# Performance work log

Hardware: AMD Instinct MI355X
Metric: run time of the kernel (lower is better)

The kernel has to match this reference:

```python
import jax, jax.numpy as jnp
import numpy as np

DIM = 192
NUM_HEADS = 6
WS = (2, 8, 8)          # (wd, wh, ww)
SHIFT = (1, 4, 4)
B, D, H, W = 2, 4, 128, 128
N_WIN_TOK = WS[0] * WS[1] * WS[2]   # 128
NW = (D // WS[0]) * (H // WS[1]) * (W // WS[2])  # 512 windows per sample


def _rel_pos_index(ws):
    d, h, w = ws
    coords = np.stack(np.meshgrid(np.arange(d), np.arange(h), np.arange(w), indexing='ij'))
    cf = coords.reshape(3, -1)
    rel = (cf[:, :, None] - cf[:, None, :]).transpose(1, 2, 0).astype(np.int64)
    rel[:, :, 0] += d - 1
    rel[:, :, 1] += h - 1
    rel[:, :, 2] += w - 1
    rel[:, :, 0] *= (2 * h - 1) * (2 * w - 1)
    rel[:, :, 1] *= 2 * w - 1
    return rel.sum(-1)  # (N, N)

REL_IDX = _rel_pos_index(WS)


def _sine_pos(HW, num_pos_feats, temperature=10000.0):
    # matches get_sine_position_encoding(normalize=True)
    scale = 2 * np.pi
    eps = 1e-6
    ones = np.ones((1, HW[0], HW[1]), np.float32)
    y = ones.cumsum(1)
    x = ones.cumsum(2)
    y = y / (y[:, -1:, :] + eps) * scale
    x = x / (x[:, :, -1:] + eps) * scale
    i = np.arange(num_pos_feats, dtype=np.float32)
    dim_t = temperature ** (2.0 * np.floor(i / 2) / num_pos_feats)
    px = x[:, :, :, None] / dim_t
    py = y[:, :, :, None] / dim_t
    px = np.stack((np.sin(px[..., 0::2]), np.cos(px[..., 1::2])), axis=4).reshape(1, HW[0], HW[1], -1)
    py = np.stack((np.sin(py[..., 0::2]), np.cos(py[..., 1::2])), axis=4).reshape(1, HW[0], HW[1], -1)
    pos = np.concatenate((py, px), axis=3)  # (1, H, W, 2*npf)
    return pos.reshape(1, HW[0] * HW[1], -1)

POS_BIAS = _sine_pos((WS[1], WS[2]), DIM // 2)  # (1, 64, DIM)


def _ln(x, w, b):
    mu = x.mean(-1, keepdims=True)
    var = x.var(-1, keepdims=True)
    return (x - mu) / jnp.sqrt(var + 1e-5) * w + b


def _qkv(x, w, b):
    B_, N, C = x.shape
    y = (x @ w.T + b).reshape(B_, N, 3, NUM_HEADS, C // NUM_HEADS).transpose(2, 0, 3, 1, 4)
    return y[0], y[1], y[2]  # each (B_, h, N, hd)


def _attn(q, k, v, mask, rpb=None):
    # q,k,v: (B_, h, N, hd); mask: (nW, N, N) or None; rpb: (h, N, N) or None
    scale = q.shape[-1] ** -0.5
    a = jnp.einsum('bhnd,bhmd->bhnm', q * scale, k)
    if rpb is not None:
        a = a + rpb[None]
    if mask is not None:
        B_, h, N, _ = a.shape
        nW = mask.shape[0]
        a = (a.reshape(B_ // nW, nW, h, N, N) + mask[None, :, None]).reshape(B_, h, N, N)
    a = jax.nn.softmax(a, axis=-1)
    out = jnp.einsum('bhnm,bhmd->bhnd', a, v)
    B_, h, N, hd = out.shape
    return out.transpose(0, 2, 1, 3).reshape(B_, N, h * hd)


def setup_inputs() -> dict:
    key = jax.random.key(0)
    ks = jax.random.split(key, 8)
    C = DIM
    hid = int(C * 2.0)
    f = lambda k, shp: jax.random.normal(k, shp, jnp.float32) * 0.02
    tbl = (2 * WS[0] - 1) * (2 * WS[1] - 1) * (2 * WS[2] - 1)
    return {
        'x': jax.random.normal(ks[0], (B, D, H, W, C), jnp.float32),
        'mask_matrix': jnp.zeros((NW, N_WIN_TOK, N_WIN_TOK), jnp.float32),
        'norm1_w': jnp.ones((C,), jnp.float32), 'norm1_b': jnp.zeros((C,), jnp.float32),
        'qkv_self_w': f(ks[1], (3 * C, C)), 'qkv_self_b': jnp.zeros((3 * C,), jnp.float32),
        'qkv_mut_w': f(ks[2], (3 * C, C)), 'qkv_mut_b': jnp.zeros((3 * C,), jnp.float32),
        'rpb_table': f(ks[3], (tbl, NUM_HEADS)),
        'proj_w': f(ks[4], (C, 2 * C)), 'proj_b': jnp.zeros((C,), jnp.float32),
        'norm2_w': jnp.ones((C,), jnp.float32), 'norm2_b': jnp.zeros((C,), jnp.float32),
        'fc11_w': f(ks[5], (hid, C)), 'fc11_b': jnp.zeros((hid,), jnp.float32),
        'fc12_w': f(ks[6], (hid, C)), 'fc12_b': jnp.zeros((hid,), jnp.float32),
        'fc2_w': f(ks[7], (C, hid)), 'fc2_b': jnp.zeros((C,), jnp.float32),
    }


def reference(x, mask_matrix, norm1_w, norm1_b, qkv_self_w, qkv_self_b,
              qkv_mut_w, qkv_mut_b, rpb_table, proj_w, proj_b,
              norm2_w, norm2_b, fc11_w, fc11_b, fc12_w, fc12_b, fc2_w, fc2_b):
    Bb, Dd, Hh, Ww_, C = x.shape
    wd, wh, ww = WS
    N = wd * wh * ww
    Nh = N // 2

    # ---- part1: windowed mutual+self attention with cyclic shift ----
    h1 = _ln(x, norm1_w, norm1_b)
    sh = jnp.roll(h1, (-SHIFT[0], -SHIFT[1], -SHIFT[2]), axis=(1, 2, 3))
    # window_partition -> (B*nW, N, C)
    xw = sh.reshape(Bb, Dd // wd, wd, Hh // wh, wh, Ww_ // ww, ww, C)
    xw = xw.transpose(0, 1, 3, 5, 2, 4, 6, 7).reshape(-1, N, C)

    # self-attention with relative position bias
    q, k, v = _qkv(xw, qkv_self_w, qkv_self_b)
    rpb = rpb_table[REL_IDX.reshape(-1)].reshape(N, N, NUM_HEADS).transpose(2, 0, 1)
    x_self = _attn(q, k, v, mask_matrix[:, :N, :N], rpb)  # (B_, N, C)

    # mutual attention (no relative bias), sine positional bias added to input
    pos = jnp.tile(jnp.asarray(POS_BIAS, x.dtype), (1, 2, 1))  # (1, N, C)
    q, k, v = _qkv(xw + pos, qkv_mut_w, qkv_mut_b)
    q1, q2 = q[:, :, :Nh], q[:, :, Nh:]
    k1, k2 = k[:, :, :Nh], k[:, :, Nh:]
    v1, v2 = v[:, :, :Nh], v[:, :, Nh:]
    m2 = mask_matrix[:, :Nh, :Nh]
    x1 = _attn(q2, k1, v1, m2)  # frame2 queries attend frame1
    x2 = _attn(q1, k2, v2, m2)
    x_out = jnp.concatenate([jnp.concatenate([x1, x2], axis=1), x_self], axis=2)  # (B_, N, 2C)
    xp = x_out @ proj_w.T + proj_b  # (B_, N, C)

    # window_reverse + roll back
    rev = xp.reshape(Bb, Dd // wd, Hh // wh, Ww_ // ww, wd, wh, ww, C)
    rev = rev.transpose(0, 1, 4, 2, 5, 3, 6, 7).reshape(Bb, Dd, Hh, Ww_, C)
    rev = jnp.roll(rev, SHIFT, axis=(1, 2, 3))
    x = x + rev

    # ---- part2: GEGLU MLP ----
    h2 = _ln(x, norm2_w, norm2_b)
    mlp = (jax.nn.gelu(h2 @ fc11_w.T + fc11_b, approximate=False) * (h2 @ fc12_w.T + fc12_b)) @ fc2_w.T + fc2_b
    return x + mlp
```

## Files before the change

kernel.cpp:

```cpp
#include <hip/hip_runtime.h>
#include <hip/hip_bf16.h>

typedef __hip_bfloat16 bf16;
typedef __attribute__((ext_vector_type(8))) short short8;
typedef __attribute__((ext_vector_type(4))) float f32x4;

#define NTOKENS 131072
#define MFMA __builtin_amdgcn_mfma_f32_16x16x32_bf16

static constexpr size_t A_OFF    = 0;
static constexpr size_t Q_OFF    = A_OFF   + (size_t)NTOKENS*192*2;
static constexpr size_t O_OFF    = Q_OFF   + (size_t)NTOKENS*576*2;
static constexpr size_t POS_OFF  = O_OFF   + (size_t)NTOKENS*384*2;
static constexpr size_t PB_OFF   = POS_OFF + (size_t)128*192*4;
static constexpr size_t RPBF_OFF = PB_OFF  + (size_t)128*576*4;
static constexpr size_t MSKF_OFF = RPBF_OFF+ (size_t)6*128*128*2;
static constexpr size_t WB_OFF   = MSKF_OFF+ (size_t)512*128*128*2;
static constexpr size_t WQS_E = 0, WQM_E = 110592, WPR_E = 221184,
                        W11_E = 294912, W12_E = 368640, W2_E = 442368, WTOT = 516096;

__device__ __forceinline__ float u2f(unsigned int ubits) {
    union { unsigned int i; float f; } c; c.i = ubits << 16; return c.f;
}
__device__ __forceinline__ unsigned pkbf(float a, float b) {
    unsigned ua = (unsigned)__bfloat16_as_ushort(__float2bfloat16(a));
    unsigned ub = (unsigned)__bfloat16_as_ushort(__float2bfloat16(b));
    return ua | (ub << 16);
}
__device__ __forceinline__ unsigned swz(unsigned b) { return b ^ (((b >> 9) & 1) << 5); }
__device__ __forceinline__ short8 u4s8(uint4 v) { union { uint4 u; short8 s; } c; c.u = v; return c.s; }

__device__ __forceinline__ void gl16(const bf16* g, void* l) {
    __builtin_amdgcn_global_load_lds(
        (const __attribute__((address_space(1))) void*)g,
        (__attribute__((address_space(3))) void*)l, 16, 0, 0);
}

__global__ __launch_bounds__(256) void cvtw_kernel(
    const float* __restrict__ a, const float* __restrict__ b, const float* __restrict__ c,
    const float* __restrict__ d, const float* __restrict__ e, const float* __restrict__ f,
    bf16* __restrict__ out) {
    int i = blockIdx.x * 256 + threadIdx.x;
    const float* src; int off;
    if      (i < (int)WQM_E) { src = a; off = (int)WQS_E; }
    else if (i < (int)WPR_E) { src = b; off = (int)WQM_E; }
    else if (i < (int)W11_E) { src = c; off = (int)WPR_E; }
    else if (i < (int)W12_E) { src = d; off = (int)W11_E; }
    else if (i < (int)W2_E)  { src = e; off = (int)W12_E; }
    else if (i < (int)WTOT)  { src = f; off = (int)W2_E; }
    else return;
    out[i] = __float2bfloat16(src[i - off]);
}

__global__ __launch_bounds__(256) void pos_kernel(float* __restrict__ pos) {
    int idx = blockIdx.x * 256 + threadIdx.x;
    if (idx >= 128 * 192) return;
    int t = idx / 192, c = idx - t * 192;
    int s = t & 63;
    int hh = s >> 3, ww = s & 7;
    const float twopi = 6.2831853071795864f;
    float coord = (c < 96) ? (float)(hh + 1) : (float)(ww + 1);
    coord = coord / (8.0f + 1e-6f) * twopi;
    int f = (c < 96) ? c : c - 96;
    float dimt = powf(10000.0f, (float)(2 * (f >> 1)) / 96.0f);
    float v = coord / dimt;
    pos[idx] = (f & 1) ? cosf(v) : sinf(v);
}

__global__ __launch_bounds__(256) void pbias_kernel(const float* __restrict__ pos,
                                                    const bf16* __restrict__ Wm,
                                                    const float* __restrict__ bqm,
                                                    float* __restrict__ PB) {
    int idx = blockIdx.x * 256 + threadIdx.x;
    if (idx >= 128 * 576) return;
    int t = idx / 576, n = idx - t * 576;
    const float* pp = pos + t * 192;
    const bf16* wp = Wm + (size_t)n * 192;
    float acc = bqm[n];
    for (int k = 0; k < 192; ++k) acc += pp[k] * __bfloat162float(wp[k]);
    PB[idx] = acc;
}

__global__ __launch_bounds__(256) void rpbF_kernel(const float* __restrict__ tbl,
                                                   bf16* __restrict__ rpbF) {
    int idx = blockIdx.x * 256 + threadIdx.x;
    if (idx >= 6 * 32 * 128 * 4) return;
    int jr = idx & 3;
    int i = (idx >> 2) & 127;
    int jq = (idx >> 9) & 31;
    int h = idx >> 14;
    int j = jq * 4 + jr;
    int di = i >> 6, hi = (i >> 3) & 7, wi = i & 7;
    int dj = j >> 6, hj = (j >> 3) & 7, wj = j & 7;
    int t = (di - dj + 1) * 225 + (hi - hj + 7) * 15 + (wi - wj + 7);
    rpbF[idx] = __float2bfloat16(tbl[t * 6 + h]);
}

__global__ __launch_bounds__(256) void mskF_kernel(const float* __restrict__ mask,
                                                   bf16* __restrict__ mskF) {
    int idx = blockIdx.x * 256 + threadIdx.x;
    int widx = idx >> 12;
    int rem = idx & 4095;
    int i = rem >> 5, jq = rem & 31;
    float4 v = *reinterpret_cast<const float4*>(mask + ((size_t)widx << 14) + i * 128 + jq * 4);
    uint2 o;
    o.x = pkbf(v.x, v.y);
    o.y = pkbf(v.z, v.w);
    *reinterpret_cast<uint2*>(mskF + ((size_t)widx << 14) + (jq * 128 + i) * 4) = o;
}

template <int PART>
__global__ __launch_bounds__(256) void ln_kernel(const float* __restrict__ xin,
                                                 const float* __restrict__ w,
                                                 const float* __restrict__ b,
                                                 bf16* __restrict__ out) {
    int tok = blockIdx.x * 4 + (threadIdx.x >> 6);
    int lane = threadIdx.x & 63;
    const float* xp = xin + (size_t)tok * 192;
    float x0 = xp[lane], x1 = xp[lane + 64], x2 = xp[lane + 128];
    float s = x0 + x1 + x2;
    float ss = x0 * x0 + x1 * x1 + x2 * x2;
    for (int off = 32; off; off >>= 1) {
        s += __shfl_xor(s, off);
        ss += __shfl_xor(ss, off);
    }
    float mean = s * (1.0f / 192.0f);
    float var = ss * (1.0f / 192.0f) - mean * mean;
    float rstd = rsqrtf(var + 1e-5f);
    size_t obase;
    if (PART) {
        int bb = tok >> 16;
        int rem = tok & 65535;
        int d = rem >> 14;
        int hw = rem & 16383;
        int hh = hw >> 7, w2 = hw & 127;
        int sd = (d + 3) & 3;
        int sh = (hh + 124) & 127;
        int sw = (w2 + 124) & 127;
        int win = ((bb * 2 + (sd >> 1)) * 16 + (sh >> 3)) * 16 + (sw >> 3);
        int t = ((sd & 1) << 6) | ((sh & 7) << 3) | (sw & 7);
        obase = ((size_t)win * 128 + t) * 192;
    } else {
        obase = (size_t)tok * 192;
    }
    out[obase + lane]       = __float2bfloat16((x0 - mean) * rstd * w[lane] + b[lane]);
    out[obase + lane + 64]  = __float2bfloat16((x1 - mean) * rstd * w[lane + 64] + b[lane + 64]);
    out[obase + lane + 128] = __float2bfloat16((x2 - mean) * rstd * w[lane + 128] + b[lane + 128]);
}

template <int MODE, int BIAS>
__global__ __launch_bounds__(256) void mgemm(
    const bf16* __restrict__ Ab, int K, int nb,
    const bf16* __restrict__ W1, const float* __restrict__ B1,
    const bf16* __restrict__ W2, const float* __restrict__ B2,
    const float* __restrict__ resid,
    void* __restrict__ outp, void* __restrict__ outp2) {
    constexpr bool DUAL = (MODE == 3 || MODE == 5);
    __shared__ __align__(16) unsigned char AsB[2][16384];
    __shared__ __align__(16) unsigned char WsB[2][8192];
    __shared__ __align__(16) unsigned char Ws2B[DUAL ? 2 : 1][DUAL ? 8192 : 16];

    int total = gridDim.x;
    int bid = blockIdx.x;
    int lin = (bid & 7) * (total >> 3) + (bid >> 3);
    int mb = lin / nb, nbk = lin - mb * nb;
    int m0 = mb << 7, n0 = nbk << 6;
    int tid = threadIdx.x;
    int w = tid >> 6, l = tid & 63;
    int wr = w >> 1, wc = w & 1;
    int lr = l & 15, lg = l >> 4;

    f32x4 acc[4][2] = {};
    f32x4 acc2[4][2] = {};

    auto stage = [&](int buf, int kc) {
        int k0 = kc << 6;
#pragma unroll
        for (int it = 0; it < 4; ++it) {
            int idx = it * 256 + tid;
            int row = idx >> 3, gs = idx & 7;
            int gsrc = gs ^ (((row >> 2) & 1) << 1);
            gl16(Ab + (size_t)(m0 + row) * K + k0 + gsrc * 8, &AsB[buf][idx * 16]);
        }
#pragma unroll
        for (int it = 0; it < 2; ++it) {
            int idx = it * 256 + tid;
            int row = idx >> 3, gs = idx & 7;
            int gsrc = gs ^ (((row >> 2) & 1) << 1);
            gl16(W1 + (size_t)(n0 + row) * K + k0 + gsrc * 8, &WsB[buf][idx * 16]);
            if (DUAL)
                gl16(W2 + (size_t)(n0 + row) * K + k0 + gsrc * 8, &Ws2B[buf][idx * 16]);
        }
    };

    int nK = K >> 6;
    stage(0, 0);
    __syncthreads();
    for (int kc = 0; kc < nK; ++kc) {
        int cur = kc & 1;
        if (kc + 1 < nK) stage(cur ^ 1, kc + 1);
        const unsigned char* as = AsB[cur];
        const unsigned char* wsb = WsB[cur];
        const unsigned char* ws2 = Ws2B[DUAL ? cur : 0];
#pragma unroll
        for (int ks = 0; ks < 2; ++ks) {
            short8 af[4], wf[2], wf2[2];
#pragma unroll
            for (int rb = 0; rb < 4; ++rb)
                af[rb] = *reinterpret_cast<const short8*>(
                    &as[swz((wr * 64 + rb * 16 + lr) * 128 + ks * 64 + lg * 16)]);
#pragma unroll
            for (int cb = 0; cb < 2; ++cb) {
                wf[cb] = *reinterpret_cast<const short8*>(
                    &wsb[swz((wc * 32 + cb * 16 + lr) * 128 + ks * 64 + lg * 16)]);
                if (DUAL)
                    wf2[cb] = *reinterpret_cast<const short8*>(
                        &ws2[swz((wc * 32 + cb * 16 + lr) * 128 + ks * 64 + lg * 16)]);
            }
#pragma unroll
            for (int rb = 0; rb < 4; ++rb)
#pragma unroll
                for (int cb = 0; cb < 2; ++cb) {
                    acc[rb][cb] = MFMA(af[rb], wf[cb], acc[rb][cb], 0, 0, 0);
                    if (DUAL) acc2[rb][cb] = MFMA(af[rb], wf2[cb], acc2[rb][cb], 0, 0, 0);
                }
        }
        __syncthreads();
    }

    if (MODE == 5) {
        bf16* eb1 = (bf16*)AsB[0];
        bf16* eb2 = (bf16*)AsB[1];
        float pbv[4][2][4];
#pragma unroll
        for (int rb = 0; rb < 4; ++rb)
#pragma unroll
            for (int r = 0; r < 4; ++r) {
                int ml = wr * 64 + rb * 16 + lg * 4 + r;
#pragma unroll
                for (int cb = 0; cb < 2; ++cb)
                    pbv[rb][cb][r] = resid[(ml & 127) * 576 + n0 + wc * 32 + cb * 16 + lr];
            }
#pragma unroll
        for (int rb = 0; rb < 4; ++rb)
#pragma unroll
            for (int r = 0; r < 4; ++r) {
                int ml = wr * 64 + rb * 16 + lg * 4 + r;
#pragma unroll
                for (int cb = 0; cb < 2; ++cb) {
                    int cl = wc * 32 + cb * 16 + lr;
                    int n = n0 + cl;
                    eb1[ml * 64 + cl] = __float2bfloat16(acc[rb][cb][r] + B1[n]);
                    eb2[ml * 64 + cl] = __float2bfloat16(acc2[rb][cb][r] + pbv[rb][cb][r]);
                }
            }
        __syncthreads();
        bf16* Og  = (bf16*)outp;
        bf16* Og2 = (bf16*)outp2;
#pragma unroll
        for (int it = 0; it < 4; ++it) {
            int idx = it * 256 + tid;
            int row = idx >> 3, g = idx & 7;
            uint4 v1 = *reinterpret_cast<const uint4*>(&eb1[row * 64 + g * 8]);
            uint4 v2 = *reinterpret_cast<const uint4*>(&eb2[row * 64 + g * 8]);
            *reinterpret_cast<uint4*>(Og  + (size_t)(m0 + row) * 576 + n0 + g * 8) = v1;
            *reinterpret_cast<uint4*>(Og2 + (size_t)(m0 + row) * 576 + n0 + g * 8) = v2;
        }
    } else if (MODE == 3) {
        bf16* eb = (bf16*)AsB[0];
#pragma unroll
        for (int rb = 0; rb < 4; ++rb)
#pragma unroll
            for (int r = 0; r < 4; ++r) {
                int ml = wr * 64 + rb * 16 + lg * 4 + r;
#pragma unroll
                for (int cb = 0; cb < 2; ++cb) {
                    int cl = wc * 32 + cb * 16 + lr;
                    int n = n0 + cl;
                    float u = acc[rb][cb][r] + B1[n];
                    float v2 = acc2[rb][cb][r] + B2[n];
                    float t = u * (0.7978845608028654f + 0.0356774081363001f * u * u);
                    float g = u * v2 / (1.0f + __expf(-2.0f * t));
                    eb[ml * 64 + cl] = __float2bfloat16(g);
                }
            }
        __syncthreads();
        bf16* Og = (bf16*)outp;
#pragma unroll
        for (int it = 0; it < 4; ++it) {
            int idx = it * 256 + tid;
            int row = idx >> 3, g = idx & 7;
            uint4 v = *reinterpret_cast<const uint4*>(&eb[row * 64 + g * 8]);
            *reinterpret_cast<uint4*>(Og + (size_t)(m0 + row) * 384 + n0 + g * 8) = v;
        }
    } else {
#pragma unroll
        for (int rb = 0; rb < 4; ++rb) {
#pragma unroll
            for (int r = 0; r < 4; ++r) {
                int m = m0 + wr * 64 + rb * 16 + lg * 4 + r;
                if (MODE == 2) {
                    int win = m >> 7, t = m & 127;
                    int bb = win >> 9, rem = win & 511;
                    int sd = ((rem >> 8) << 1) | (t >> 6);
                    int sh = (((rem >> 4) & 15) << 3) | ((t >> 3) & 7);
                    int sw = ((rem & 15) << 3) | (t & 7);
                    int dq = (sd + 1) & 3;
                    int hq = (sh + 4) & 127;
                    int wq = (sw + 4) & 127;
                    size_t gb = ((((size_t)bb * 4 + dq) * 128 + hq) * 128 + wq) * 192;
                    float* Rr = (float*)outp;
#pragma unroll
                    for (int cb = 0; cb < 2; ++cb) {
                        int n = n0 + wc * 32 + cb * 16 + lr;
                        Rr[gb + n] = resid[gb + n] + acc[rb][cb][r] + B1[n];
                    }
                } else {
                    float* Og = (float*)outp;
#pragma unroll
                    for (int cb = 0; cb < 2; ++cb) {
                        int n = n0 + wc * 32 + cb * 16 + lr;
                        Og[(size_t)m * 192 + n] =
                            resid[(size_t)m * 192 + n] + acc[rb][cb][r] + B1[n];
                    }
                }
            }
        }
    }
}

__global__ __launch_bounds__(256) void attn_self(
    const bf16* __restrict__ Qb, const bf16* __restrict__ rpbF,
    const bf16* __restrict__ mskF, bf16* __restrict__ Ob, int b2) {
    __shared__ __align__(16) bf16 VtB[4096];
    __shared__ __align__(16) bf16 EpiB[4][1280];
    int bid = blockIdx.x;
    int lin = (bid & 7) * 384 + (bid >> 3);
    int widx = lin / 6, h = lin - widx * 6;
    int win = b2 * 512 + widx;
    int tid = threadIdx.x, w = tid >> 6, l = tid & 63;
    int lr = l & 15, lg = l >> 4;
    const float qscale = 0.17677669529663689f;
    size_t qbase = (size_t)widx * 128 * 576 + h * 32;

#pragma unroll
    for (int it = 0; it < 16; ++it) {
        int idx = it * 256 + tid;
        int d = idx & 31, j = idx >> 5;
        bf16 v = Qb[qbase + (size_t)j * 576 + 384 + d];
        VtB[(d * 256 + (((j >> 3) ^ (d & 7)) << 4) + (j & 7) * 2) >> 1] = v;
    }

    uint4 kf[8], qf[2];
#pragma unroll
    for (int jb = 0; jb < 8; ++jb)
        kf[jb] = *reinterpret_cast<const uint4*>(Qb + qbase + (size_t)(jb * 16 + lr) * 576 + 192 + lg * 8);
    int i0 = w * 32;
#pragma unroll
    for (int ib = 0; ib < 2; ++ib)
        qf[ib] = *reinterpret_cast<const uint4*>(Qb + qbase + (size_t)(i0 + ib * 16 + lr) * 576 + lg * 8);
    f32x4 s[8][2] = {};
#pragma unroll
    for (int jb = 0; jb < 8; ++jb)
#pragma unroll
        for (int ib = 0; ib < 2; ++ib)
            s[jb][ib] = MFMA(u4s8(kf[jb]), u4s8(qf[ib]), s[jb][ib], 0, 0, 0);

    const bf16* rpF = rpbF + (size_t)h * 16384;
    const bf16* mpF = mskF + (size_t)widx * 16384;
#pragma unroll
    for (int jb = 0; jb < 8; ++jb) {
        int jq0 = jb * 4 + lg;
#pragma unroll
        for (int ib = 0; ib < 2; ++ib) {
            int il = i0 + ib * 16 + lr;
            uint2 rv = *reinterpret_cast<const uint2*>(rpF + (jq0 * 128 + il) * 4);
            uint2 mv = *reinterpret_cast<const uint2*>(mpF + (jq0 * 128 + il) * 4);
            s[jb][ib][0] = fmaf(s[jb][ib][0], qscale, u2f(rv.x & 0xffffu) + u2f(mv.x & 0xffffu));
            s[jb][ib][1] = fmaf(s[jb][ib][1], qscale, u2f(rv.x >> 16) + u2f(mv.x >> 16));
            s[jb][ib][2] = fmaf(s[jb][ib][2], qscale, u2f(rv.y & 0xffffu) + u2f(mv.y & 0xffffu));
            s[jb][ib][3] = fmaf(s[jb][ib][3], qscale, u2f(rv.y >> 16) + u2f(mv.y >> 16));
        }
    }

    float rs[2];
    unsigned w0[2][8], w1[2][8];
#pragma unroll
    for (int ib = 0; ib < 2; ++ib) {
        float mx = -1e30f;
#pragma unroll
        for (int jb = 0; jb < 8; ++jb)
#pragma unroll
            for (int r = 0; r < 4; ++r) mx = fmaxf(mx, s[jb][ib][r]);
        mx = fmaxf(mx, __shfl_xor(mx, 16));
        mx = fmaxf(mx, __shfl_xor(mx, 32));
        float sum = 0.0f;
#pragma unroll
        for (int jb = 0; jb < 8; ++jb)
#pragma unroll
            for (int r = 0; r < 4; ++r) {
                float e = __expf(s[jb][ib][r] - mx);
                s[jb][ib][r] = e;
                sum += e;
            }
        sum += __shfl_xor(sum, 16);
        sum += __shfl_xor(sum, 32);
        rs[ib] = 1.0f / sum;
#pragma unroll
        for (int jb = 0; jb < 8; ++jb) {
            w0[ib][jb] = pkbf(s[jb][ib][0], s[jb][ib][1]);
            w1[ib][jb] = pkbf(s[jb][ib][2], s[jb][ib][3]);
        }
    }
    __syncthreads();

    f32x4 o[2][2] = {};
    int srcA = lr + 16 * (2 * (lg & 1));
    int srcB = srcA + 16;
    bool hi = ((lg >> 1) & 1) != 0;
#pragma unroll
    for (int ks = 0; ks < 4; ++ks) {
        short8 vt[2];
#pragma unroll
        for (int db = 0; db < 2; ++db) {
            int d = db * 16 + lr;
            vt[db] = *reinterpret_cast<const short8*>(
                &VtB[(d * 256 + (((ks * 4 + lg) ^ (d & 7)) << 4)) >> 1]);
        }
#pragma unroll
        for (int ib = 0; ib < 2; ++ib) {
            unsigned xa0 = (unsigned)__shfl((int)w0[ib][2 * ks], srcA, 64);
            unsigned xa1 = (unsigned)__shfl((int)w0[ib][2 * ks + 1], srcA, 64);
            unsigned xb0 = (unsigned)__shfl((int)w1[ib][2 * ks], srcA, 64);
            unsigned xb1 = (unsigned)__shfl((int)w1[ib][2 * ks + 1], srcA, 64);
            unsigned xc0 = (unsigned)__shfl((int)w0[ib][2 * ks], srcB, 64);
            unsigned xc1 = (unsigned)__shfl((int)w0[ib][2 * ks + 1], srcB, 64);
            unsigned xd0 = (unsigned)__shfl((int)w1[ib][2 * ks], srcB, 64);
            unsigned xd1 = (unsigned)__shfl((int)w1[ib][2 * ks + 1], srcB, 64);
            uint4 bfv;
            bfv.x = hi ? xa1 : xa0;
            bfv.y = hi ? xb1 : xb0;
            bfv.z = hi ? xc1 : xc0;
            bfv.w = hi ? xd1 : xd0;
            short8 pb = u4s8(bfv);
#pragma unroll
            for (int db = 0; db < 2; ++db) o[db][ib] = MFMA(vt[db], pb, o[db][ib], 0, 0, 0);
        }
    }

    bf16* eb = &EpiB[w][0];
#pragma unroll
    for (int db = 0; db < 2; ++db)
#pragma unroll
        for (int ib = 0; ib < 2; ++ib)
#pragma unroll
            for (int r = 0; r < 4; ++r) {
                int d = db * 16 + lg * 4 + r;
                int il = ib * 16 + lr;
                eb[il * 40 + d] = __float2bfloat16(o[db][ib][r] * rs[ib]);
            }
    int il2 = l >> 1, hf = l & 1;
    uint4 oa = *reinterpret_cast<const uint4*>(&eb[il2 * 40 + hf * 16]);
    uint4 ob2 = *reinterpret_cast<const uint4*>(&eb[il2 * 40 + hf * 16 + 8]);
    size_t gbase = ((size_t)win * 128 + i0 + il2) * 384 + 192 + h * 32 + hf * 16;
    *reinterpret_cast<uint4*>(Ob + gbase) = oa;
    *reinterpret_cast<uint4*>(Ob + gbase + 8) = ob2;
}

__global__ __launch_bounds__(256) void attn_mut(
    const bf16* __restrict__ Qb, const bf16* __restrict__ mskF, bf16* __restrict__ Ob,
    int b2) {
    __shared__ __align__(16) bf16 VtB[4096];
    __shared__ __align__(16) bf16 EpiB[4][1280];
    int bid = blockIdx.x;
    int lin = (bid & 7) * 384 + (bid >> 3);
    int widx = lin / 6, h = lin - widx * 6;
    int win = b2 * 512 + widx;
    int tid = threadIdx.x, w = tid >> 6, l = tid & 63;
    int lr = l & 15, lg = l >> 4;
    const float qscale = 0.17677669529663689f;
    size_t qbase = (size_t)widx * 128 * 576 + h * 32;

#pragma unroll
    for (int it = 0; it < 16; ++it) {
        int idx = it * 256 + tid;
        int d = idx & 31, j = idx >> 5;
        bf16 v = Qb[qbase + (size_t)j * 576 + 384 + d];
        VtB[(d * 256 + (((j >> 3) ^ (d & 7)) << 4) + (j & 7) * 2) >> 1] = v;
    }

    int i0 = w * 32;
    int qoff = (w < 2) ? 64 : -64;
    int koff = (w < 2) ? 0 : 64;
    uint4 kf[4], qf[2];
#pragma unroll
    for (int jb = 0; jb < 4; ++jb)
        kf[jb] = *reinterpret_cast<const uint4*>(
            Qb + qbase + (size_t)(koff + jb * 16 + lr) * 576 + 192 + lg * 8);
#pragma unroll
    for (int ib = 0; ib < 2; ++ib)
        qf[ib] = *reinterpret_cast<const uint4*>(
            Qb + qbase + (size_t)(i0 + ib * 16 + lr + qoff) * 576 + lg * 8);
    f32x4 s[4][2] = {};
#pragma unroll
    for (int jb = 0; jb < 4; ++jb)
#pragma unroll
        for (int ib = 0; ib < 2; ++ib)
            s[jb][ib] = MFMA(u4s8(kf[jb]), u4s8(qf[ib]), s[jb][ib], 0, 0, 0);

    const bf16* mpF = mskF + (size_t)widx * 16384;
    int ibase = (i0 & 63);
#pragma unroll
    for (int jb = 0; jb < 4; ++jb) {
        int jq0 = jb * 4 + lg;
#pragma unroll
        for (int ib = 0; ib < 2; ++ib) {
            int il = ibase + ib * 16 + lr;
            uint2 mv = *reinterpret_cast<const uint2*>(mpF + (jq0 * 128 + il) * 4);
            s[jb][ib][0] = fmaf(s[jb][ib][0], qscale, u2f(mv.x & 0xffffu));
            s[jb][ib][1] = fmaf(s[jb][ib][1], qscale, u2f(mv.x >> 16));
            s[jb][ib][2] = fmaf(s[jb][ib][2], qscale, u2f(mv.y & 0xffffu));
            s[jb][ib][3] = fmaf(s[jb][ib][3], qscale, u2f(mv.y >> 16));
        }
    }

    float rs[2];
    unsigned w0[2][4], w1[2][4];
#pragma unroll
    for (int ib = 0; ib < 2; ++ib) {
        float mx = -1e30f;
#pragma unroll
        for (int jb = 0; jb < 4; ++jb)
#pragma unroll
            for (int r = 0; r < 4; ++r) mx = fmaxf(mx, s[jb][ib][r]);
        mx = fmaxf(mx, __shfl_xor(mx, 16));
        mx = fmaxf(mx, __shfl_xor(mx, 32));
        float sum = 0.0f;
#pragma unroll
        for (int jb = 0; jb < 4; ++jb)
#pragma unroll
            for (int r = 0; r < 4; ++r) {
                float e = __expf(s[jb][ib][r] - mx);
                s[jb][ib][r] = e;
                sum += e;
            }
        sum += __shfl_xor(sum, 16);
        sum += __shfl_xor(sum, 32);
        rs[ib] = 1.0f / sum;
#pragma unroll
        for (int jb = 0; jb < 4; ++jb) {
            w0[ib][jb] = pkbf(s[jb][ib][0], s[jb][ib][1]);
            w1[ib][jb] = pkbf(s[jb][ib][2], s[jb][ib][3]);
        }
    }
    __syncthreads();

    f32x4 o[2][2] = {};
    int srcA = lr + 16 * (2 * (lg & 1));
    int srcB = srcA + 16;
    bool hi = ((lg >> 1) & 1) != 0;
    int gb0 = koff >> 3;
#pragma unroll
    for (int ks = 0; ks < 2; ++ks) {
        short8 vt[2];
#pragma unroll
        for (int db = 0; db < 2; ++db) {
            int d = db * 16 + lr;
            vt[db] = *reinterpret_cast<const short8*>(
                &VtB[(d * 256 + (((gb0 + ks * 4 + lg) ^ (d & 7)) << 4)) >> 1]);
        }
#pragma unroll
        for (int ib = 0; ib < 2; ++ib) {
            unsigned xa0 = (unsigned)__shfl((int)w0[ib][2 * ks], srcA, 64);
            unsigned xa1 = (unsigned)__shfl((int)w0[ib][2 * ks + 1], srcA, 64);
            unsigned xb0 = (unsigned)__shfl((int)w1[ib][2 * ks], srcA, 64);
            unsigned xb1 = (unsigned)__shfl((int)w1[ib][2 * ks + 1], srcA, 64);
            unsigned xc0 = (unsigned)__shfl((int)w0[ib][2 * ks], srcB, 64);
            unsigned xc1 = (unsigned)__shfl((int)w0[ib][2 * ks + 1], srcB, 64);
            unsigned xd0 = (unsigned)__shfl((int)w1[ib][2 * ks], srcB, 64);
            unsigned xd1 = (unsigned)__shfl((int)w1[ib][2 * ks + 1], srcB, 64);
            uint4 bfv;
            bfv.x = hi ? xa1 : xa0;
            bfv.y = hi ? xb1 : xb0;
            bfv.z = hi ? xc1 : xc0;
            bfv.w = hi ? xd1 : xd0;
            short8 pb = u4s8(bfv);
#pragma unroll
            for (int db = 0; db < 2; ++db) o[db][ib] = MFMA(vt[db], pb, o[db][ib], 0, 0, 0);
        }
    }

    bf16* eb = &EpiB[w][0];
#pragma unroll
    for (int db = 0; db < 2; ++db)
#pragma unroll
        for (int ib = 0; ib < 2; ++ib)
#pragma unroll
            for (int r = 0; r < 4; ++r) {
                int d = db * 16 + lg * 4 + r;
                int il = ib * 16 + lr;
                eb[il * 40 + d] = __float2bfloat16(o[db][ib][r] * rs[ib]);
            }
    int il2 = l >> 1, hf = l & 1;
    uint4 oa = *reinterpret_cast<const uint4*>(&eb[il2 * 40 + hf * 16]);
    uint4 ob2 = *reinterpret_cast<const uint4*>(&eb[il2 * 40 + hf * 16 + 8]);
    size_t gbase = ((size_t)win * 128 + i0 + il2) * 384 + h * 32 + hf * 16;
    *reinterpret_cast<uint4*>(Ob + gbase) = oa;
    *reinterpret_cast<uint4*>(Ob + gbase + 8) = ob2;
}

extern "C" void kernel_launch(void* const* d_in, const int* in_sizes, int n_in,
                              void* d_out, int out_size, void* d_ws, size_t ws_size,
                              hipStream_t stream) {
    const float* x    = (const float*)d_in[0];
    const float* mask = (const float*)d_in[1];
    const float* n1w  = (const float*)d_in[2];
    const float* n1b  = (const float*)d_in[3];
    const float* wqs  = (const float*)d_in[4];
    const float* bqs  = (const float*)d_in[5];
    const float* wqm  = (const float*)d_in[6];
    const float* bqm  = (const float*)d_in[7];
    const float* rpbt = (const float*)d_in[8];
    const float* wproj= (const float*)d_in[9];
    const float* bproj= (const float*)d_in[10];
    const float* n2w  = (const float*)d_in[11];
    const float* n2b  = (const float*)d_in[12];
    const float* w11  = (const float*)d_in[13];
    const float* b11  = (const float*)d_in[14];
    const float* w12  = (const float*)d_in[15];
    const float* b12  = (const float*)d_in[16];
    const float* w2   = (const float*)d_in[17];
    const float* b2   = (const float*)d_in[18];

    char* ws = (char*)d_ws;
    bf16*  A    = (bf16*)(ws + A_OFF);
    bf16*  Q    = (bf16*)(ws + Q_OFF);
    bf16*  O    = (bf16*)(ws + O_OFF);
    float* pos  = (float*)(ws + POS_OFF);
    float* PB   = (float*)(ws + PB_OFF);
    bf16*  rpbF = (bf16*)(ws + RPBF_OFF);
    bf16*  mskF = (bf16*)(ws + MSKF_OFF);
    bf16*  WB   = (bf16*)(ws + WB_OFF);
    bf16*  Hb = A;
    bf16*  G  = Q;
    float* R  = (float*)d_out;
    float* out = (float*)d_out;
    bf16*  Q2 = (bf16*)d_out;

    cvtw_kernel<<<(WTOT + 255) / 256, 256, 0, stream>>>(wqs, wqm, wproj, w11, w12, w2, WB);
    pos_kernel<<<96, 256, 0, stream>>>(pos);
    pbias_kernel<<<288, 256, 0, stream>>>(pos, WB + WQM_E, bqm, PB);
    rpbF_kernel<<<384, 256, 0, stream>>>(rpbt, rpbF);
    mskF_kernel<<<8192, 256, 0, stream>>>(mask, mskF);
    ln_kernel<1><<<32768, 256, 0, stream>>>(x, n1w, n1b, A);

    for (int hf = 0; hf < 2; ++hf) {
        const bf16* Ah = A + (size_t)hf * 65536 * 192;
        bf16* Qh = Q + (size_t)hf * 65536 * 576;
        mgemm<5, 0><<<9 * 512, 256, 0, stream>>>(Ah, 192, 9, WB + WQS_E, bqs, WB + WQM_E,
                                                 nullptr, PB, Qh, Q2);
        attn_self<<<3072, 256, 0, stream>>>(Qh, rpbF, mskF, O, hf);
        attn_mut<<<3072, 256, 0, stream>>>(Q2, mskF, O, hf);
    }

    mgemm<2, 0><<<3 * 1024, 256, 0, stream>>>(O, 384, 3, WB + WPR_E, bproj, nullptr, nullptr,
                                              x, R, nullptr);
    ln_kernel<0><<<32768, 256, 0, stream>>>(R, n2w, n2b, Hb);
    mgemm<3, 0><<<6 * 1024, 256, 0, stream>>>(Hb, 192, 6, WB + W11_E, b11, WB + W12_E, b12,
                                              nullptr, G, nullptr);
    mgemm<4, 0><<<3 * 1024, 256, 0, stream>>>(G, 384, 3, WB + W2_E, b2, nullptr, nullptr,
                                              R, out, nullptr);
}
```

Measured before the change: 565.9 us.

## Halve GEMM K-chunk to 32 and shrink shared memory for higher occupancy

Changes the mgemm K tile from 64 to 32 and packs the double buffers into one shared-memory pool, replacing the old swizzle with an XOR swizzle sized for 64-byte rows. It also adds a minimum-blocks hint to launch_bounds so more workgroups can be resident per CU. The goal is to hide memory latency through occupancy. The cost is twice as many K iterations and barriers, each doing less MFMA work, plus possible register spills caused by the occupancy hint.

After: 623.7 us. 1.1x slower.

```diff
diff --git a/kernel.cpp b/kernel.cpp
--- a/kernel.cpp
+++ b/kernel.cpp
@@ -27,7 +27,6 @@
     unsigned ub = (unsigned)__bfloat16_as_ushort(__float2bfloat16(b));
     return ua | (ub << 16);
 }
-__device__ __forceinline__ unsigned swz(unsigned b) { return b ^ (((b >> 9) & 1) << 5); }
 __device__ __forceinline__ short8 u4s8(uint4 v) { union { uint4 u; short8 s; } c; c.u = v; return c.s; }
 
 __device__ __forceinline__ void gl16(const bf16* g, void* l) {
@@ -149,16 +148,18 @@
 }
 
 template <int MODE, int BIAS>
-__global__ __launch_bounds__(256) void mgemm(
+__global__ __launch_bounds__(256, (MODE == 3 || MODE == 5) ? 5 : 6) void mgemm(
     const bf16* __restrict__ Ab, int K, int nb,
     const bf16* __restrict__ W1, const float* __restrict__ B1,
     const bf16* __restrict__ W2, const float* __restrict__ B2,
     const float* __restrict__ resid,
     void* __restrict__ outp, void* __restrict__ outp2) {
     constexpr bool DUAL = (MODE == 3 || MODE == 5);
-    __shared__ __align__(16) unsigned char AsB[2][16384];
-    __shared__ __align__(16) unsigned char WsB[2][8192];
-    __shared__ __align__(16) unsigned char Ws2B[DUAL ? 2 : 1][DUAL ? 8192 : 16];
+    constexpr int POOLSZ = DUAL ? 32768 : 24576;
+    __shared__ __align__(16) unsigned char pool[POOLSZ];
+    unsigned char* As  = pool;
+    unsigned char* Wsb = pool + 16384;
+    unsigned char* Ws2 = DUAL ? (pool + 24576) : (pool + 16384);
 
     int total = gridDim.x;
     int bid = blockIdx.x;
@@ -174,63 +175,60 @@
     f32x4 acc2[4][2] = {};
 
     auto stage = [&](int buf, int kc) {
-        int k0 = kc << 6;
-#pragma unroll
-        for (int it = 0; it < 4; ++it) {
-            int idx = it * 256 + tid;
-            int row = idx >> 3, gs = idx & 7;
-            int gsrc = gs ^ (((row >> 2) & 1) << 1);
-            gl16(Ab + (size_t)(m0 + row) * K + k0 + gsrc * 8, &AsB[buf][idx * 16]);
-        }
+        int k0 = kc << 5;
 #pragma unroll
         for (int it = 0; it < 2; ++it) {
             int idx = it * 256 + tid;
-            int row = idx >> 3, gs = idx & 7;
-            int gsrc = gs ^ (((row >> 2) & 1) << 1);
-            gl16(W1 + (size_t)(n0 + row) * K + k0 + gsrc * 8, &WsB[buf][idx * 16]);
+            int row = idx >> 2, gs = idx & 3;
+            int gsrc = gs ^ ((row >> 1) & 3);
+            gl16(Ab + (size_t)(m0 + row) * K + k0 + gsrc * 8, As + buf * 8192 + idx * 16);
+        }
+        {
+            int row = tid >> 2, gs = tid & 3;
+            int gsrc = gs ^ ((row >> 1) & 3);
+            gl16(W1 + (size_t)(n0 + row) * K + k0 + gsrc * 8, Wsb + buf * 4096 + tid * 16);
             if (DUAL)
-                gl16(W2 + (size_t)(n0 + row) * K + k0 + gsrc * 8, &Ws2B[buf][idx * 16]);
+                gl16(W2 + (size_t)(n0 + row) * K + k0 + gsrc * 8, Ws2 + buf * 4096 + tid * 16);
         }
     };
 
-    int nK = K >> 6;
+    int nK = K >> 5;
     stage(0, 0);
     __syncthreads();
     for (int kc = 0; kc < nK; ++kc) {
         int cur = kc & 1;
         if (kc + 1 < nK) stage(cur ^ 1, kc + 1);
-        const unsigned char* as = AsB[cur];
-        const unsigned char* wsb = WsB[cur];
-        const unsigned char* ws2 = Ws2B[DUAL ? cur : 0];
-#pragma unroll
-        for (int ks = 0; ks < 2; ++ks) {
-            short8 af[4], wf[2], wf2[2];
-#pragma unroll
-            for (int rb = 0; rb < 4; ++rb)
-                af[rb] = *reinterpret_cast<const short8*>(
-                    &as[swz((wr * 64 + rb * 16 + lr) * 128 + ks * 64 + lg * 16)]);
+        const unsigned char* as  = As  + cur * 8192;
+        const unsigned char* wsb = Wsb + cur * 4096;
+        const unsigned char* ws2 = Ws2 + cur * 4096;
+        short8 af[4], wf[2], wf2[2];
+#pragma unroll
+        for (int rb = 0; rb < 4; ++rb) {
+            int row = wr * 64 + rb * 16 + lr;
+            af[rb] = *reinterpret_cast<const short8*>(
+                &as[row * 64 + ((lg ^ ((row >> 1) & 3)) << 4)]);
+        }
+#pragma unroll
+        for (int cb = 0; cb < 2; ++cb) {
+            int row = wc * 32 + cb * 16 + lr;
+            unsigned off = row * 64 + ((lg ^ ((row >> 1) & 3)) << 4);
+            wf[cb] = *reinterpret_cast<const short8*>(&wsb[off]);
+            if (DUAL)
+                wf2[cb] = *reinterpret_cast<const short8*>(&ws2[off]);
+        }
+#pragma unroll
+        for (int rb = 0; rb < 4; ++rb)
 #pragma unroll
             for (int cb = 0; cb < 2; ++cb) {
-                wf[cb] = *reinterpret_cast<const short8*>(
-                    &wsb[swz((wc * 32 + cb * 16 + lr) * 128 + ks * 64 + lg * 16)]);
-                if (DUAL)
-                    wf2[cb] = *reinterpret_cast<const short8*>(
-                        &ws2[swz((wc * 32 + cb * 16 + lr) * 128 + ks * 64 + lg * 16)]);
-            }
-#pragma unroll
-            for (int rb = 0; rb < 4; ++rb)
-#pragma unroll
-                for (int cb = 0; cb < 2; ++cb) {
-                    acc[rb][cb] = MFMA(af[rb], wf[cb], acc[rb][cb], 0, 0, 0);
-                    if (DUAL) acc2[rb][cb] = MFMA(af[rb], wf2[cb], acc2[rb][cb], 0, 0, 0);
-                }
-        }
+                acc[rb][cb] = MFMA(af[rb], wf[cb], acc[rb][cb], 0, 0, 0);
+                if (DUAL) acc2[rb][cb] = MFMA(af[rb], wf2[cb], acc2[rb][cb], 0, 0, 0);
+            }
         __syncthreads();
     }
 
     if (MODE == 5) {
-        bf16* eb1 = (bf16*)AsB[0];
-        bf16* eb2 = (bf16*)AsB[1];
+        bf16* eb1 = (bf16*)pool;
+        bf16* eb2 = (bf16*)(pool + 16384);
         float pbv[4][2][4];
 #pragma unroll
         for (int rb = 0; rb < 4; ++rb)
@@ -267,7 +265,7 @@
             *reinterpret_cast<uint4*>(Og2 + (size_t)(m0 + row) * 576 + n0 + g * 8) = v2;
         }
     } else if (MODE == 3) {
-        bf16* eb = (bf16*)AsB[0];
+        bf16* eb = (bf16*)pool;
 #pragma unroll
         for (int rb = 0; rb < 4; ++rb)
 #pragma unroll
```
